# Performance work log

Measured on AMD Instinct MI355X. Metric: run time of the kernel, lower is better.

## Reference

```python
import jax, jax.numpy as jnp
import numpy as np

N_SUB = 8  # fixed RK4 substeps per output interval (stands in for torchdiffeq's adaptive dopri5 at rtol=1e-5)


def setup_inputs() -> dict:
    key = jax.random.key(0)
    k = jax.random.split(key, 7)
    B, D, H, O, T = 16384, 64, 256, 32, 50
    y0 = jax.random.normal(k[0], (B, D), dtype=jnp.float32)
    t = jnp.arange(T, dtype=jnp.float32)
    W1 = jax.random.normal(k[1], (D, H), dtype=jnp.float32) / np.float32(np.sqrt(D))
    b1 = jnp.zeros((H,), dtype=jnp.float32)
    W2 = jax.random.normal(k[2], (H, D), dtype=jnp.float32) / np.float32(np.sqrt(H))
    b2 = jnp.zeros((D,), dtype=jnp.float32)
    Wfc = jax.random.normal(k[3], (D, O), dtype=jnp.float32) / np.float32(np.sqrt(D))
    bfc = jnp.zeros((O,), dtype=jnp.float32)
    return {"y0": y0, "t": t, "W1": W1, "b1": b1, "W2": W2, "b2": b2, "Wfc": Wfc, "bfc": bfc}


def reference(y0, t, W1, b1, W2, b2, Wfc, bfc):
    # odefunc: 2-layer tanh MLP, autonomous dynamics f(y)
    def f(y):
        return jnp.tanh(y @ W1 + b1) @ W2 + b2

    def rk4_step(y, h):
        k1 = f(y)
        k2 = f(y + 0.5 * h * k1)
        k3 = f(y + 0.5 * h * k2)
        k4 = f(y + h * k3)
        return y + (h / 6.0) * (k1 + 2.0 * k2 + 2.0 * k3 + k4)

    def interval(y, dt):
        h = dt / N_SUB
        def sub(yc, _):
            return rk4_step(yc, h), None
        y, _ = jax.lax.scan(sub, y, None, length=N_SUB)
        return y, y

    dts = t[1:] - t[:-1]            # [T-1]
    _, ys = jax.lax.scan(interval, y0, dts)  # [T-1, B, D]
    sol = jnp.concatenate([y0[None], ys], axis=0)  # [T, B, D]
    # final linear projection fc
    return sol @ Wfc + bfc          # [T, B, O]
```

## Files before the change

kernel.cpp:

```cpp
#include <hip/hip_runtime.h>


typedef _Float16 f16;
typedef _Float16 f16x4 __attribute__((ext_vector_type(4)));
typedef _Float16 f16x8 __attribute__((ext_vector_type(8)));
typedef float    f32x4 __attribute__((ext_vector_type(4)));

#define MFMA(a, b, c) __builtin_amdgcn_mfma_f32_16x16x32_f16((a), (b), (c), 0, 0, 0)

static __device__ __forceinline__ float fast_tanh(float x) {
    float e = __builtin_amdgcn_exp2f(x * 2.885390081777927f);
    float r = __builtin_amdgcn_rcpf(e + 1.0f);
    return __builtin_fmaf(-2.0f, r, 1.0f);
}

static __device__ __forceinline__ void split4(float t0, float t1, float t2, float t3,
                                              f16x4* hv, f16x4* lv) {
    auto h01 = __builtin_amdgcn_cvt_pkrtz(t0, t1);
    auto h23 = __builtin_amdgcn_cvt_pkrtz(t2, t3);
    float l0 = t0 - (float)h01[0], l1 = t1 - (float)h01[1];
    float l2 = t2 - (float)h23[0], l3 = t3 - (float)h23[1];
    auto s01 = __builtin_amdgcn_cvt_pkrtz(l0, l1);
    auto s23 = __builtin_amdgcn_cvt_pkrtz(l2, l3);
    f16x4 h, l;
    h[0] = h01[0]; h[1] = h01[1]; h[2] = h23[0]; h[3] = h23[1];
    l[0] = s01[0]; l[1] = s01[1]; l[2] = s23[0]; l[3] = s23[1];
    *hv = h; *lv = l;
}

__global__ __launch_bounds__(512, 2) void node_fused(
    const float* __restrict__ y0g, const float* __restrict__ tg,
    const float* __restrict__ W1,  const float* __restrict__ b1,
    const float* __restrict__ W2,  const float* __restrict__ b2,
    const float* __restrict__ Wfc, const float* __restrict__ bfc,
    float* __restrict__ out)
{
    __shared__ __align__(16) f16 w1loL[16 * 2 * 64 * 8];
    __shared__ __align__(16) f16 w2loL[4 * 8 * 64 * 8];
    __shared__ __align__(16) f16 wfcL [2 * 2 * 64 * 8];
    __shared__ __align__(16) f16 hhiB[4 * 16 * 264];
    __shared__ __align__(16) f16 hloB[4 * 16 * 264];
    __shared__ __align__(16) f16 khiB[4 * 16 * 72];
    __shared__ __align__(16) f16 kloB[4 * 16 * 72];

    const int tid  = (int)threadIdx.x;
    const int wid  = tid >> 6;
    const int lane = tid & 63;
    const int q    = lane >> 4;
    const int c    = lane & 15;
    const int pair = wid >> 1;
    const int half = wid & 1;
    const int R0   = (int)blockIdx.x * 64 + pair * 16;
    const int jt0  = half * 8;
    const int dt0  = half * 2;

    f16* __restrict__ hhi = &hhiB[pair * 16 * 264];
    f16* __restrict__ hlo = &hloB[pair * 16 * 264];
    f16* __restrict__ khi = &khiB[pair * 16 * 72];
    f16* __restrict__ klo = &kloB[pair * 16 * 72];

    f16x8 w1a[8][2];
#pragma unroll
    for (int j = 0; j < 8; ++j)
#pragma unroll
        for (int ks = 0; ks < 2; ++ks)
#pragma unroll
            for (int jj = 0; jj < 8; ++jj)
                w1a[j][ks][jj] = (f16)W1[(ks * 32 + q * 8 + jj) * 256 + (jt0 + j) * 16 + c];

    f16x8 w2a[2][8];
#pragma unroll
    for (int d = 0; d < 2; ++d)
#pragma unroll
        for (int ks = 0; ks < 8; ++ks)
#pragma unroll
            for (int jj = 0; jj < 8; ++jj)
                w2a[d][ks][jj] = (f16)W2[(ks * 32 + q * 8 + jj) * 64 + (dt0 + d) * 16 + c];

    for (int jr = 0; jr < 2; ++jr) {
        int jt = wid * 2 + jr;
        for (int ks = 0; ks < 2; ++ks)
            for (int j = 0; j < 8; ++j) {
                float w = W1[(ks * 32 + q * 8 + j) * 256 + jt * 16 + c];
                f16 hi = (f16)w;
                w1loL[((jt * 2 + ks) * 64 + lane) * 8 + j] = (f16)(w - (float)hi);
            }
    }
    {
        int dt = wid >> 1;
        for (int kr = 0; kr < 4; ++kr) {
            int ks = (wid & 1) * 4 + kr;
            for (int j = 0; j < 8; ++j) {
                float w = W2[(ks * 32 + q * 8 + j) * 64 + dt * 16 + c];
                f16 hi = (f16)w;
                w2loL[((dt * 8 + ks) * 64 + lane) * 8 + j] = (f16)(w - (float)hi);
            }
        }
    }
    if (wid == 0)
        for (int ot = 0; ot < 2; ++ot)
            for (int ks = 0; ks < 2; ++ks)
                for (int j = 0; j < 8; ++j)
                    wfcL[((ot * 2 + ks) * 64 + lane) * 8 + j] =
                        (f16)Wfc[(ks * 32 + q * 8 + j) * 32 + ot * 16 + c];
    __syncthreads();

    f32x4 b2v[2], bfcv;
#pragma unroll
    for (int d = 0; d < 2; ++d)
#pragma unroll
        for (int r = 0; r < 4; ++r) b2v[d][r] = b2[(dt0 + d) * 16 + 4 * q + r];
#pragma unroll
    for (int r = 0; r < 4; ++r) bfcv[r] = bfc[half * 16 + 4 * q + r];

    f16x8 y0hi[2], y0lo[2];
#pragma unroll
    for (int ks = 0; ks < 2; ++ks)
#pragma unroll
        for (int j = 0; j < 8; ++j) {
            float v = y0g[(R0 + c) * 64 + ks * 32 + q * 8 + j];
            f16 hi = (f16)v;
            y0hi[ks][j] = hi;
            y0lo[ks][j] = (f16)(v - (float)hi);
        }

    f32x4 P1[8];
#pragma unroll
    for (int j = 0; j < 8; ++j) {
        f32x4 cc;
#pragma unroll
        for (int r = 0; r < 4; ++r) cc[r] = b1[(jt0 + j) * 16 + 4 * q + r];
#pragma unroll
        for (int ks = 0; ks < 2; ++ks) {
            f16x8 alo = *reinterpret_cast<const f16x8*>(&w1loL[(((jt0 + j) * 2 + ks) * 64 + lane) * 8]);
            cc = MFMA(w1a[j][ks], y0hi[ks], cc);
            cc = MFMA(w1a[j][ks], y0lo[ks], cc);
            cc = MFMA(alo,        y0hi[ks], cc);
        }
        P1[j] = cc;
    }
    f32x4 pfc;
    {
        f32x4 z = {0.f, 0.f, 0.f, 0.f};
#pragma unroll
        for (int ks = 0; ks < 2; ++ks) {
            f16x8 wa = *reinterpret_cast<const f16x8*>(&wfcL[((half * 2 + ks) * 64 + lane) * 8]);
            z = MFMA(wa, y0hi[ks], z);
            z = MFMA(wa, y0lo[ks], z);
        }
        pfc = z;
    }
    {
        f32x4 v = pfc + bfcv;
        *reinterpret_cast<f32x4*>(&out[(size_t)(R0 + c) * 32 + half * 16 + 4 * q]) = v;
    }

    f32x4 ksum[2], dy[2];
#pragma unroll
    for (int d = 0; d < 2; ++d) dy[d] = f32x4{0.f, 0.f, 0.f, 0.f};

#pragma unroll
    for (int j = 0; j < 8; ++j) {
        float t0 = fast_tanh(P1[j][0]), t1 = fast_tanh(P1[j][1]);
        float t2 = fast_tanh(P1[j][2]), t3 = fast_tanh(P1[j][3]);
        f16x4 hv, lv;
        split4(t0, t1, t2, t3, &hv, &lv);
        *reinterpret_cast<f16x4*>(&hhi[c * 264 + (jt0 + j) * 16 + 4 * q]) = hv;
        *reinterpret_cast<f16x4*>(&hlo[c * 264 + (jt0 + j) * 16 + 4 * q]) = lv;
    }
    __syncthreads();

    float hh = 0.f, ch = 0.f, c6 = 0.f;

    auto gemm2half = [&](float w, bool first, bool last) {
        f32x4 ka[2];
#pragma unroll
        for (int d = 0; d < 2; ++d) ka[d] = b2v[d];
#pragma unroll
        for (int ks = 0; ks < 8; ++ks) {
            f16x8 bhi = *reinterpret_cast<const f16x8*>(&hhi[c * 264 + ks * 32 + q * 8]);
            f16x8 blo = *reinterpret_cast<const f16x8*>(&hlo[c * 264 + ks * 32 + q * 8]);
#pragma unroll
            for (int d = 0; d < 2; ++d) {
                f16x8 alo = *reinterpret_cast<const f16x8*>(&w2loL[(((dt0 + d) * 8 + ks) * 64 + lane) * 8]);
                ka[d] = MFMA(w2a[d][ks], bhi, ka[d]);
                ka[d] = MFMA(w2a[d][ks], blo, ka[d]);
                ka[d] = MFMA(alo,        bhi, ka[d]);
            }
        }
#pragma unroll
        for (int d = 0; d < 2; ++d) {
            if (first)      ksum[d] = ka[d];
            else            ksum[d] += ka[d] * w;
            f32x4 kv;
            if (!last) {
                kv = ka[d];
            } else {
                kv = ksum[d] * c6;
                dy[d] += kv;
            }
            f16x4 hv, lv;
            split4(kv[0], kv[1], kv[2], kv[3], &hv, &lv);
            *reinterpret_cast<f16x4*>(&khi[c * 72 + (dt0 + d) * 16 + 4 * q]) = hv;
            *reinterpret_cast<f16x4*>(&klo[c * 72 + (dt0 + d) * 16 + 4 * q]) = lv;
        }
        __syncthreads();
    };

    auto gemm1half = [&](float carg, bool fin) {
        f16x8 kh0 = *reinterpret_cast<const f16x8*>(&khi[c * 72 + q * 8]);
        f16x8 kh1 = *reinterpret_cast<const f16x8*>(&khi[c * 72 + 32 + q * 8]);
        f16x8 kl0 = *reinterpret_cast<const f16x8*>(&klo[c * 72 + q * 8]);
        f16x8 kl1 = *reinterpret_cast<const f16x8*>(&klo[c * 72 + 32 + q * 8]);
#pragma unroll
        for (int j = 0; j < 8; ++j) {
            int jt = jt0 + j;
            f16x8 a0 = *reinterpret_cast<const f16x8*>(&w1loL[((jt * 2 + 0) * 64 + lane) * 8]);
            f16x8 a1 = *reinterpret_cast<const f16x8*>(&w1loL[((jt * 2 + 1) * 64 + lane) * 8]);
            f32x4 z = {0.f, 0.f, 0.f, 0.f};
            z = MFMA(w1a[j][0], kh0, z);
            z = MFMA(w1a[j][0], kl0, z);
            z = MFMA(a0,        kh0, z);
            z = MFMA(w1a[j][1], kh1, z);
            z = MFMA(w1a[j][1], kl1, z);
            z = MFMA(a1,        kh1, z);
            float a0f, a1f, a2f, a3f;
            if (fin) {
                P1[j] += z;
                a0f = P1[j][0]; a1f = P1[j][1]; a2f = P1[j][2]; a3f = P1[j][3];
            } else {
                a0f = __builtin_fmaf(carg, z[0], P1[j][0]);
                a1f = __builtin_fmaf(carg, z[1], P1[j][1]);
                a2f = __builtin_fmaf(carg, z[2], P1[j][2]);
                a3f = __builtin_fmaf(carg, z[3], P1[j][3]);
            }
            float t0 = fast_tanh(a0f), t1 = fast_tanh(a1f);
            float t2 = fast_tanh(a2f), t3 = fast_tanh(a3f);
            f16x4 hv, lv;
            split4(t0, t1, t2, t3, &hv, &lv);
            *reinterpret_cast<f16x4*>(&hhi[c * 264 + jt * 16 + 4 * q]) = hv;
            *reinterpret_cast<f16x4*>(&hlo[c * 264 + jt * 16 + 4 * q]) = lv;
        }
        __syncthreads();
    };

#pragma unroll 1
    for (int ti = 0; ti < 49; ++ti) {
        float dtv = tg[ti + 1] - tg[ti];
        hh = dtv * 0.125f;
        ch = 0.5f * hh;
        c6 = hh * (1.0f / 6.0f);
#pragma unroll 1
        for (int sub = 0; sub < 8; ++sub) {
            gemm2half(1.0f, true,  false);
            gemm1half(ch, false);
            gemm2half(2.0f, false, false);
            gemm1half(ch, false);
            gemm2half(2.0f, false, false);
            gemm1half(hh, false);
            gemm2half(1.0f, false, true);
            gemm1half(0.0f, true);
        }
#pragma unroll
        for (int d = 0; d < 2; ++d) {
            f16x4 hv, lv;
            split4(dy[d][0], dy[d][1], dy[d][2], dy[d][3], &hv, &lv);
            *reinterpret_cast<f16x4*>(&khi[c * 72 + (dt0 + d) * 16 + 4 * q]) = hv;
            *reinterpret_cast<f16x4*>(&klo[c * 72 + (dt0 + d) * 16 + 4 * q]) = lv;
            dy[d] = f32x4{0.f, 0.f, 0.f, 0.f};
        }
        __syncthreads();
        {
            f16x8 dh0 = *reinterpret_cast<const f16x8*>(&khi[c * 72 + q * 8]);
            f16x8 dh1 = *reinterpret_cast<const f16x8*>(&khi[c * 72 + 32 + q * 8]);
            f16x8 dl0 = *reinterpret_cast<const f16x8*>(&klo[c * 72 + q * 8]);
            f16x8 dl1 = *reinterpret_cast<const f16x8*>(&klo[c * 72 + 32 + q * 8]);
            f16x8 wa0 = *reinterpret_cast<const f16x8*>(&wfcL[((half * 2 + 0) * 64 + lane) * 8]);
            f16x8 wa1 = *reinterpret_cast<const f16x8*>(&wfcL[((half * 2 + 1) * 64 + lane) * 8]);
            pfc = MFMA(wa0, dh0, pfc);
            pfc = MFMA(wa0, dl0, pfc);
            pfc = MFMA(wa1, dh1, pfc);
            pfc = MFMA(wa1, dl1, pfc);
        }
        __syncthreads();
        size_t base = (size_t)(ti + 1) * (16384 * 32);
        {
            f32x4 v = pfc + bfcv;
            *reinterpret_cast<f32x4*>(&out[base + (size_t)(R0 + c) * 32 + half * 16 + 4 * q]) = v;
        }
    }
}

extern "C" void kernel_launch(void* const* d_in, const int* in_sizes, int n_in,
                              void* d_out, int out_size, void* d_ws, size_t ws_size,
                              hipStream_t stream) {
    (void)in_sizes; (void)n_in; (void)d_ws; (void)ws_size; (void)out_size;
    const float* y0  = (const float*)d_in[0];
    const float* t   = (const float*)d_in[1];
    const float* W1  = (const float*)d_in[2];
    const float* b1  = (const float*)d_in[3];
    const float* W2  = (const float*)d_in[4];
    const float* b2  = (const float*)d_in[5];
    const float* Wfc = (const float*)d_in[6];
    const float* bfc = (const float*)d_in[7];
    float* out = (float*)d_out;
    node_fused<<<dim3(256), dim3(512), 0, stream>>>(y0, t, W1, b1, W2, b2, Wfc, bfc, out);
}
```

Measured before the change: 4.878 ms.

## Skew two warp groups by one phase to overlap GEMM stages across block halves

Replaces the nested interval/substep loops with one flat phase loop. Warps 4-7 (g=1) start one phase earlier than warps 0-3 (g=0), so at any moment the two halves of the block are in different stages (GEMM1 vs GEMM2 or epilogue). The aim is to mix tanh/VALU-heavy and MFMA-heavy phases across the SIMDs instead of every warp hitting the same bottleneck in lockstep. Each group's pairs use their own shared buffers, so the skew stays legal. It adds one extra barrier iteration plus per-phase branching and state-machine overhead.

```diff
diff --git a/kernel.cpp b/kernel.cpp
--- a/kernel.cpp
+++ b/kernel.cpp
@@ -50,6 +50,7 @@
     const int c    = lane & 15;
     const int pair = wid >> 1;
     const int half = wid & 1;
+    const int g    = wid >> 2;
     const int R0   = (int)blockIdx.x * 64 + pair * 16;
     const int jt0  = half * 8;
     const int dt0  = half * 2;
@@ -170,9 +171,13 @@
     }
     __syncthreads();
 
-    float hh = 0.f, ch = 0.f, c6 = 0.f;
-
-    auto gemm2half = [&](float w, bool first, bool last) {
+    int   ti = 0, r = 0;
+    float dtv = tg[1] - tg[0];
+    float hh  = dtv * 0.125f;
+    float ch  = 0.5f * hh;
+    float c6  = hh * (1.0f / 6.0f);
+
+    auto gemm2body = [&](float w, bool first, bool last) {
         f32x4 ka[2];
 #pragma unroll
         for (int d = 0; d < 2; ++d) ka[d] = b2v[d];
@@ -204,10 +209,9 @@
             *reinterpret_cast<f16x4*>(&khi[c * 72 + (dt0 + d) * 16 + 4 * q]) = hv;
             *reinterpret_cast<f16x4*>(&klo[c * 72 + (dt0 + d) * 16 + 4 * q]) = lv;
         }
-        __syncthreads();
     };
 
-    auto gemm1half = [&](float carg, bool fin) {
+    auto gemm1body = [&](float carg, bool fin) {
         f16x8 kh0 = *reinterpret_cast<const f16x8*>(&khi[c * 72 + q * 8]);
         f16x8 kh1 = *reinterpret_cast<const f16x8*>(&khi[c * 72 + 32 + q * 8]);
         f16x8 kl0 = *reinterpret_cast<const f16x8*>(&klo[c * 72 + q * 8]);
@@ -241,26 +245,9 @@
             *reinterpret_cast<f16x4*>(&hhi[c * 264 + jt * 16 + 4 * q]) = hv;
             *reinterpret_cast<f16x4*>(&hlo[c * 264 + jt * 16 + 4 * q]) = lv;
         }
-        __syncthreads();
     };
 
-#pragma unroll 1
-    for (int ti = 0; ti < 49; ++ti) {
-        float dtv = tg[ti + 1] - tg[ti];
-        hh = dtv * 0.125f;
-        ch = 0.5f * hh;
-        c6 = hh * (1.0f / 6.0f);
-#pragma unroll 1
-        for (int sub = 0; sub < 8; ++sub) {
-            gemm2half(1.0f, true,  false);
-            gemm1half(ch, false);
-            gemm2half(2.0f, false, false);
-            gemm1half(ch, false);
-            gemm2half(2.0f, false, false);
-            gemm1half(hh, false);
-            gemm2half(1.0f, false, true);
-            gemm1half(0.0f, true);
-        }
+    auto epiA = [&]() {
 #pragma unroll
         for (int d = 0; d < 2; ++d) {
             f16x4 hv, lv;
@@ -269,25 +256,56 @@
             *reinterpret_cast<f16x4*>(&klo[c * 72 + (dt0 + d) * 16 + 4 * q]) = lv;
             dy[d] = f32x4{0.f, 0.f, 0.f, 0.f};
         }
+    };
+
+    auto epiB = [&]() {
+        f16x8 dh0 = *reinterpret_cast<const f16x8*>(&khi[c * 72 + q * 8]);
+        f16x8 dh1 = *reinterpret_cast<const f16x8*>(&khi[c * 72 + 32 + q * 8]);
+        f16x8 dl0 = *reinterpret_cast<const f16x8*>(&klo[c * 72 + q * 8]);
+        f16x8 dl1 = *reinterpret_cast<const f16x8*>(&klo[c * 72 + 32 + q * 8]);
+        f16x8 wa0 = *reinterpret_cast<const f16x8*>(&wfcL[((half * 2 + 0) * 64 + lane) * 8]);
+        f16x8 wa1 = *reinterpret_cast<const f16x8*>(&wfcL[((half * 2 + 1) * 64 + lane) * 8]);
+        pfc = MFMA(wa0, dh0, pfc);
+        pfc = MFMA(wa0, dl0, pfc);
+        pfc = MFMA(wa1, dh1, pfc);
+        pfc = MFMA(wa1, dl1, pfc);
+        size_t base = (size_t)(ti + 1) * (16384 * 32);
+        f32x4 v = pfc + bfcv;
+        *reinterpret_cast<f32x4*>(&out[base + (size_t)(R0 + c) * 32 + half * 16 + 4 * q]) = v;
+    };
+
+    const int TOTAL = 49 * 66;
+#pragma unroll 1
+    for (int gp = 0; gp < TOTAL + 1; ++gp) {
+        bool active = g ? (gp < TOTAL) : (gp >= 1);
+        if (active) {
+            if (r < 64) {
+                int st = r & 7;
+                int i  = st >> 1;
+                if ((st & 1) == 0) {
+                    float w = (i == 1 || i == 2) ? 2.0f : 1.0f;
+                    gemm2body(w, i == 0, i == 3);
+                } else {
+                    float carg = (i < 2) ? ch : (i == 2 ? hh : 0.0f);
+                    gemm1body(carg, i == 3);
+                }
+            } else if (r == 64) {
+                epiA();
+            } else {
+                epiB();
+            }
+            ++r;
+            if (r == 66) {
+                r = 0; ++ti;
+                if (ti < 49) {
+                    float d2 = tg[ti + 1] - tg[ti];
+                    hh = d2 * 0.125f;
+                    ch = 0.5f * hh;
+                    c6 = hh * (1.0f / 6.0f);
+                }
+            }
+        }
         __syncthreads();
-        {
-            f16x8 dh0 = *reinterpret_cast<const f16x8*>(&khi[c * 72 + q * 8]);
-            f16x8 dh1 = *reinterpret_cast<const f16x8*>(&khi[c * 72 + 32 + q * 8]);
-            f16x8 dl0 = *reinterpret_cast<const f16x8*>(&klo[c * 72 + q * 8]);
-            f16x8 dl1 = *reinterpret_cast<const f16x8*>(&klo[c * 72 + 32 + q * 8]);
-            f16x8 wa0 = *reinterpret_cast<const f16x8*>(&wfcL[((half * 2 + 0) * 64 + lane) * 8]);
-            f16x8 wa1 = *reinterpret_cast<const f16x8*>(&wfcL[((half * 2 + 1) * 64 + lane) * 8]);
-            pfc = MFMA(wa0, dh0, pfc);
-            pfc = MFMA(wa0, dl0, pfc);
-            pfc = MFMA(wa1, dh1, pfc);
-            pfc = MFMA(wa1, dl1, pfc);
-        }
-        __syncthreads();
-        size_t base = (size_t)(ti + 1) * (16384 * 32);
-        {
-            f32x4 v = pfc + bfcv;
-            *reinterpret_cast<f32x4*>(&out[base + (size_t)(R0 + c) * 32 + half * 16 + 4 * q]) = v;
-        }
     }
 }
 
```

Measured after the change: 6.409 ms. 31.4% more time.
